# Performance work log

Hardware: AMD Instinct MI355X
Metric: run time of the kernel (lower is better)

Reference implementation:

```python
import jax, jax.numpy as jnp
import numpy as np

V_CNT = 10000
B = 16
N = B * V_CNT          # total nodes
K = 6                  # Chebyshev order
CH = [3, 128, 64, 32, 128]
G = 8                  # GroupNorm groups (divides 128, 64, 32)
EPS = 1e-5
AVG_DEG = 16


def setup_inputs() -> dict:
    key = jax.random.key(0)
    ks = jax.random.split(key, 8)
    n_edges = N * AVG_DEG
    inp = {
        "x": jax.random.normal(ks[0], (N, CH[0]), jnp.float32),
        "edge_index": jax.random.randint(ks[1], (2, n_edges), 0, N, jnp.int32).astype(jnp.int64),
    }
    for l in range(3):
        cin, cout = CH[l], CH[l + 1]
        s = (1.0 / (cin * K)) ** 0.5
        inp[f"W{l}"] = jax.random.uniform(ks[2 + l], (K, cin, cout), jnp.float32, -s, s)
        inp[f"b{l}"] = jnp.zeros((cout,), jnp.float32)
        inp[f"gamma{l}"] = jnp.ones((cout,), jnp.float32)
        inp[f"beta{l}"] = jnp.zeros((cout,), jnp.float32)
    din = V_CNT * CH[3]
    s = (1.0 / din) ** 0.5
    inp["W_last"] = jax.random.uniform(ks[5], (din, CH[4]), jnp.float32, -s, s)
    inp["b_last"] = jnp.zeros((CH[4],), jnp.float32)
    return inp


def _cheb_edge_weights(edge_index):
    # PyG ChebConv sym normalization with lambda_max=2: L_hat = L - I = -D^{-1/2} A D^{-1/2}
    row, col = edge_index[0], edge_index[1]
    deg = jax.ops.segment_sum(jnp.ones(row.shape, jnp.float32), row, num_segments=N)
    dis = jnp.where(deg > 0, jax.lax.rsqrt(jnp.maximum(deg, 1.0)), 0.0)  # deg^{-1/2}, inf->0
    return -dis[row] * dis[col], row, col


def _cheb_conv(x, row, col, w, W, b):
    # Chebyshev recursion: Tx0=x, Tx1=L_hat x, Tx_k = 2 L_hat Tx_{k-1} - Tx_{k-2}
    prop = lambda h: jax.ops.segment_sum(w[:, None] * h[col], row, num_segments=N)
    Tx0 = x
    out = Tx0 @ W[0]
    Tx1 = prop(Tx0)
    out = out + Tx1 @ W[1]
    for k in range(2, W.shape[0]):
        Tx2 = 2.0 * prop(Tx1) - Tx0
        out = out + Tx2 @ W[k]
        Tx0, Tx1 = Tx1, Tx2
    return out + b


def _group_norm(h, gamma, beta):
    n, C = h.shape
    hg = h.reshape(n, G, C // G)
    mu = hg.mean(axis=2, keepdims=True)
    var = hg.var(axis=2, keepdims=True)
    hg = (hg - mu) * jax.lax.rsqrt(var + EPS)
    return hg.reshape(n, C) * gamma + beta


def reference(x, edge_index, W0, b0, gamma0, beta0, W1, b1, gamma1, beta1,
              W2, b2, gamma2, beta2, W_last, b_last):
    w, row, col = _cheb_edge_weights(edge_index)
    Ws = [W0, W1, W2]
    bs = [b0, b1, b2]
    gs = [gamma0, gamma1, gamma2]
    betas = [beta0, beta1, beta2]
    h = x
    for l in range(3):
        h = _cheb_conv(h, row, col, w, Ws[l], bs[l])
        h = _group_norm(h, gs[l], betas[l])
        h = jax.nn.relu(h)
    h = h.reshape(-1, V_CNT * CH[3])  # [B, v_cnt*32]
    return h @ W_last + b_last
```

## Files before the change

kernel.cpp:

```cpp
#include <hip/hip_runtime.h>
#include <hip/hip_fp16.h>


#define NN 160000
#define EE 2560000
#define FD2 256

typedef __attribute__((ext_vector_type(8))) _Float16 half8;
typedef __attribute__((ext_vector_type(4))) float floatx4;

__device__ inline float2 h2f2(unsigned u) {
  __half2 h = __builtin_bit_cast(__half2, u);
  return __half22float2(h);
}
__device__ inline unsigned short f2h(float f) {
  return __builtin_bit_cast(unsigned short, __float2half_rn(f));
}
__device__ inline unsigned packh2(float a, float b) {
  return __builtin_bit_cast(unsigned, __floats2half2_rn(a, b));
}

__global__ __launch_bounds__(256) void k_zero(int* __restrict__ p, int n) {
  int i = blockIdx.x * 256 + threadIdx.x;
  if (i < n) p[i] = 0;
}

__global__ __launch_bounds__(256) void k_hist(const int* __restrict__ ei, int* __restrict__ deg) {
  int e = blockIdx.x * 256 + threadIdx.x;
  if (e < EE) atomicAdd(&deg[ei[e]], 1);
}

__global__ __launch_bounds__(256) void k_dis(const int* __restrict__ deg, float* __restrict__ dis) {
  int i = blockIdx.x * 256 + threadIdx.x;
  if (i < NN) { int d = deg[i]; dis[i] = d > 0 ? rsqrtf((float)d) : 0.f; }
}

__global__ __launch_bounds__(256) void k_scan1(const int* __restrict__ deg, int* __restrict__ rowStart,
                                               int* __restrict__ bsum) {
  __shared__ int s[256];
  int tid = threadIdx.x;
  int i = blockIdx.x * 256 + tid;
  int v = deg[i];
  s[tid] = v;
  __syncthreads();
  for (int off = 1; off < 256; off <<= 1) {
    int t = (tid >= off) ? s[tid - off] : 0;
    __syncthreads();
    s[tid] += t;
    __syncthreads();
  }
  rowStart[i] = s[tid] - v;
  if (tid == 255) bsum[blockIdx.x] = s[255];
}

__global__ void k_scan2(int* __restrict__ bsum, int nb) {
  __shared__ int s[1024];
  int tid = threadIdx.x;
  int v = (tid < nb) ? bsum[tid] : 0;
  s[tid] = v;
  __syncthreads();
  for (int off = 1; off < 1024; off <<= 1) {
    int t = (tid >= off) ? s[tid - off] : 0;
    __syncthreads();
    s[tid] += t;
    __syncthreads();
  }
  if (tid < nb) bsum[tid] = s[tid] - v;
}

__global__ __launch_bounds__(256) void k_scan3(int* __restrict__ rowStart, const int* __restrict__ bsum) {
  int i = blockIdx.x * 256 + threadIdx.x;
  rowStart[i] += bsum[blockIdx.x];
  if (i == 0) rowStart[NN] = EE;
}

__global__ __launch_bounds__(256) void k_scatter(const int* __restrict__ ei, const int* __restrict__ rowStart,
                                                 int* __restrict__ cursor, const float* __restrict__ dis,
                                                 int2* __restrict__ ew) {
  int e = blockIdx.x * 256 + threadIdx.x;
  if (e >= EE) return;
  int r = ei[e];
  int c = ei[EE + e];
  int pos = rowStart[r] + atomicAdd(&cursor[r], 1);
  ew[pos] = make_int2(c, __float_as_int(-dis[r] * dis[c]));
}

__global__ __launch_bounds__(256) void k_copyx(const float* __restrict__ x, float* __restrict__ A,
                                               unsigned short* __restrict__ TxAll) {
  int i = blockIdx.x * 256 + threadIdx.x;
  if (i < NN * 3) {
    float v = x[i];
    A[i] = v;
    int node = i / 3, c = i - node * 3;
    TxAll[node * 32 + c] = f2h(v);
  }
}

template <int MODE>
__global__ __launch_bounds__(256) void k_prop3(const float* __restrict__ Tsrc, float* __restrict__ Tdst,
                                               unsigned short* __restrict__ TxAll, int ks,
                                               const int* __restrict__ rowStart, const int2* __restrict__ ew) {
  int i = blockIdx.x * 256 + threadIdx.x;
  if (i >= NN) return;
  float a0 = 0.f, a1 = 0.f, a2 = 0.f;
  int e = rowStart[i], e1 = rowStart[i + 1];
  for (; e + 3 < e1; e += 4) {
    int2 p0 = ew[e], p1 = ew[e + 1], p2 = ew[e + 2], p3 = ew[e + 3];
    float w0 = __int_as_float(p0.y), w1 = __int_as_float(p1.y);
    float w2 = __int_as_float(p2.y), w3 = __int_as_float(p3.y);
    a0 += w0 * Tsrc[p0.x * 3] + w1 * Tsrc[p1.x * 3] + w2 * Tsrc[p2.x * 3] + w3 * Tsrc[p3.x * 3];
    a1 += w0 * Tsrc[p0.x * 3 + 1] + w1 * Tsrc[p1.x * 3 + 1] + w2 * Tsrc[p2.x * 3 + 1] + w3 * Tsrc[p3.x * 3 + 1];
    a2 += w0 * Tsrc[p0.x * 3 + 2] + w1 * Tsrc[p1.x * 3 + 2] + w2 * Tsrc[p2.x * 3 + 2] + w3 * Tsrc[p3.x * 3 + 2];
  }
  for (; e < e1; e++) {
    int2 p0 = ew[e];
    float w0 = __int_as_float(p0.y);
    a0 += w0 * Tsrc[p0.x * 3];
    a1 += w0 * Tsrc[p0.x * 3 + 1];
    a2 += w0 * Tsrc[p0.x * 3 + 2];
  }
  if (MODE == 2) {
    a0 = 2.f * a0 - Tdst[i * 3];
    a1 = 2.f * a1 - Tdst[i * 3 + 1];
    a2 = 2.f * a2 - Tdst[i * 3 + 2];
  }
  Tdst[i * 3] = a0; Tdst[i * 3 + 1] = a1; Tdst[i * 3 + 2] = a2;
  unsigned short* tp = TxAll + i * 32 + ks * 3;
  tp[0] = f2h(a0); tp[1] = f2h(a1); tp[2] = f2h(a2);
}

__global__ __launch_bounds__(256) void k_padW0(const float* __restrict__ W0, unsigned short* __restrict__ Bt) {
  int idx = blockIdx.x * 256 + threadIdx.x;
  if (idx >= 128 * 32) return;
  int co = idx >> 5, t = idx & 31;
  Bt[co * 32 + t] = (t < 18) ? f2h(W0[t * 128 + co]) : (unsigned short)0;
}

template <int CIN, int COUT>
__global__ __launch_bounds__(256) void k_combine(const float* __restrict__ W, unsigned short* __restrict__ Bt) {
  int idx = blockIdx.x * 256 + threadIdx.x;
  if (idx >= CIN * 6 * COUT) return;
  int co = idx % COUT;
  int j  = (idx / COUT) % 6;
  int ci = idx / (6 * COUT);
  float c0, c1, c2, c3, c4, c5;
  switch (j) {
    case 0:  c0 = 1;  c1 = 0;  c2 = -1; c3 = 0;   c4 = 1;  c5 = 0;   break;
    case 1:  c0 = 0;  c1 = 1;  c2 = 0;  c3 = -3;  c4 = 0;  c5 = 5;   break;
    case 2:  c0 = 0;  c1 = 0;  c2 = 2;  c3 = 0;   c4 = -8; c5 = 0;   break;
    case 3:  c0 = 0;  c1 = 0;  c2 = 0;  c3 = 4;   c4 = 0;  c5 = -20; break;
    case 4:  c0 = 0;  c1 = 0;  c2 = 0;  c3 = 0;   c4 = 8;  c5 = 0;   break;
    default: c0 = 0;  c1 = 0;  c2 = 0;  c3 = 0;   c4 = 0;  c5 = 16;  break;
  }
  float s = 0.f;
  s += c0 * W[(0 * CIN + ci) * COUT + co];
  s += c1 * W[(1 * CIN + ci) * COUT + co];
  s += c2 * W[(2 * CIN + ci) * COUT + co];
  s += c3 * W[(3 * CIN + ci) * COUT + co];
  s += c4 * W[(4 * CIN + ci) * COUT + co];
  s += c5 * W[(5 * CIN + ci) * COUT + co];
  Bt[(j * COUT + co) * CIN + ci] = f2h(s);
}

template <int KDIM, int COUT>
__global__ __launch_bounds__(256) void k_gemm(const unsigned short* __restrict__ A,
                                              const unsigned short* __restrict__ Bt,
                                              unsigned short* __restrict__ Y) {
  constexpr int KP = KDIM + 8;
  __shared__ unsigned short As[64 * KP];
  __shared__ unsigned short Bs[64 * KP];
  int i0 = blockIdx.x * 64;
  int c0 = blockIdx.y * 64;
  for (int idx = threadIdx.x; idx < 64 * (KDIM / 8); idx += 256) {
    int row = idx / (KDIM / 8), seg = idx % (KDIM / 8);
    uint4 v = ((const uint4*)A)[(size_t)(i0 + row) * (KDIM / 8) + seg];
    *reinterpret_cast<uint4*>(&As[row * KP + seg * 8]) = v;
  }
  for (int idx = threadIdx.x; idx < 64 * (KDIM / 8); idx += 256) {
    int row = idx / (KDIM / 8), seg = idx % (KDIM / 8);
    uint4 v = ((const uint4*)Bt)[(size_t)(c0 + row) * (KDIM / 8) + seg];
    *reinterpret_cast<uint4*>(&Bs[row * KP + seg * 8]) = v;
  }
  __syncthreads();
  int w = threadIdx.x >> 6, lane = threadIdx.x & 63;
  int mn = lane & 15, q = lane >> 4;
  floatx4 acc[4];
#pragma unroll
  for (int cb = 0; cb < 4; cb++) acc[cb] = {0.f, 0.f, 0.f, 0.f};
#pragma unroll
  for (int ks = 0; ks < KDIM / 32; ks++) {
    half8 af = *reinterpret_cast<const half8*>(&As[(16 * w + mn) * KP + ks * 32 + q * 8]);
#pragma unroll
    for (int cb = 0; cb < 4; cb++) {
      half8 bf = *reinterpret_cast<const half8*>(&Bs[(cb * 16 + mn) * KP + ks * 32 + q * 8]);
      acc[cb] = __builtin_amdgcn_mfma_f32_16x16x32_f16(af, bf, acc[cb], 0, 0, 0);
    }
  }
#pragma unroll
  for (int cb = 0; cb < 4; cb++) {
    int jc = c0 + cb * 16 + mn;
    int slice = jc / COUT, cc = jc % COUT;
    unsigned short* dst = Y + (size_t)slice * NN * COUT + cc;
#pragma unroll
    for (int r = 0; r < 4; r++) {
      int i = i0 + 16 * w + q * 4 + r;
      dst[(size_t)i * COUT] = f2h(acc[cb][r]);
    }
  }
}

template <int CPN>
__global__ __launch_bounds__(256) void k_horner(const unsigned* __restrict__ Ysrc, unsigned* __restrict__ Ydst,
                                                const int* __restrict__ rowStart, const int2* __restrict__ ew) {
  int t = blockIdx.x * 256 + threadIdx.x;
  int i = t / CPN;
  int cp = t % CPN;
  float2 a = h2f2(Ydst[(size_t)i * CPN + cp]);
  float acc0 = a.x, acc1 = a.y;
  int e = rowStart[i], e1 = rowStart[i + 1];
  for (; e + 7 < e1; e += 8) {
    int2 p[8];
    unsigned u[8];
#pragma unroll
    for (int k = 0; k < 8; k++) p[k] = ew[e + k];
#pragma unroll
    for (int k = 0; k < 8; k++) u[k] = Ysrc[(size_t)p[k].x * CPN + cp];
#pragma unroll
    for (int k = 0; k < 8; k++) {
      float w = __int_as_float(p[k].y);
      float2 f = h2f2(u[k]);
      acc0 += w * f.x;
      acc1 += w * f.y;
    }
  }
  for (; e < e1; e++) {
    int2 p0 = ew[e];
    float w0 = __int_as_float(p0.y);
    float2 f0 = h2f2(Ysrc[(size_t)p0.x * CPN + cp]);
    acc0 += w0 * f0.x;
    acc1 += w0 * f0.y;
  }
  Ydst[(size_t)i * CPN + cp] = packh2(acc0, acc1);
}

template <int CPG>
__global__ __launch_bounds__(256) void k_gn(const unsigned short* __restrict__ src, const float* __restrict__ bias,
                                            const float* __restrict__ gamma, const float* __restrict__ beta,
                                            unsigned short* __restrict__ dst) {
  constexpr int C = CPG * 8;
  int t = blockIdx.x * 256 + threadIdx.x;
  int i = t >> 3, g = t & 7;
  float v[CPG];
  const unsigned* p = reinterpret_cast<const unsigned*>(src + (size_t)i * C + g * CPG);
#pragma unroll
  for (int q = 0; q < CPG / 2; q++) {
    float2 f = h2f2(p[q]);
    v[2 * q] = f.x; v[2 * q + 1] = f.y;
  }
  float mean = 0.f;
#pragma unroll
  for (int c = 0; c < CPG; c++) { v[c] += bias[g * CPG + c]; mean += v[c]; }
  mean *= (1.f / CPG);
  float var = 0.f;
#pragma unroll
  for (int c = 0; c < CPG; c++) { float d = v[c] - mean; var += d * d; }
  var *= (1.f / CPG);
  float rs = rsqrtf(var + 1e-5f);
  unsigned* dp = reinterpret_cast<unsigned*>(dst + (size_t)i * C + g * CPG);
#pragma unroll
  for (int q = 0; q < CPG / 2; q++) {
    float o0 = fmaxf((v[2 * q] - mean) * rs * gamma[g * CPG + 2 * q] + beta[g * CPG + 2 * q], 0.f);
    float o1 = fmaxf((v[2 * q + 1] - mean) * rs * gamma[g * CPG + 2 * q + 1] + beta[g * CPG + 2 * q + 1], 0.f);
    dp[q] = packh2(o0, o1);
  }
}

__global__ __launch_bounds__(256) void k_final1(const unsigned short* __restrict__ h3,
                                                const float* __restrict__ Wl,
                                                float* __restrict__ part) {
  __shared__ float hs[16 * FD2];
  __shared__ float red[2048];
  int d0 = blockIdx.x * FD2;
  const unsigned* h3u = reinterpret_cast<const unsigned*>(h3);
  for (int idx = threadIdx.x; idx < 16 * (FD2 / 2); idx += 256) {
    int b = idx / (FD2 / 2), dq = idx % (FD2 / 2);
    float2 f = h2f2(h3u[(size_t)b * 160000 + (d0 >> 1) + dq]);
    hs[b * FD2 + 2 * dq] = f.x;
    hs[b * FD2 + 2 * dq + 1] = f.y;
  }
  __syncthreads();
  int w = threadIdx.x >> 6, lane = threadIdx.x & 63;
  float a0[16], a1[16];
#pragma unroll
  for (int b = 0; b < 16; b++) { a0[b] = 0.f; a1[b] = 0.f; }
  const float* wp = Wl + (size_t)(d0 + w * (FD2 / 4)) * 128 + 2 * lane;
#pragma unroll 2
  for (int r = 0; r < FD2 / 4; r++) {
    float2 wv = *reinterpret_cast<const float2*>(wp + (size_t)r * 128);
    int row = w * (FD2 / 4) + r;
#pragma unroll
    for (int b = 0; b < 16; b++) {
      float h = hs[b * FD2 + row];
      a0[b] += wv.x * h;
      a1[b] += wv.y * h;
    }
  }
  float2* red2 = reinterpret_cast<float2*>(red);
  for (int ww = 0; ww < 4; ww++) {
    if (w == ww) {
#pragma unroll
      for (int b = 0; b < 16; b++) {
        if (ww == 0) {
          red2[b * 64 + lane] = make_float2(a0[b], a1[b]);
        } else {
          float2 r2 = red2[b * 64 + lane];
          r2.x += a0[b]; r2.y += a1[b];
          red2[b * 64 + lane] = r2;
        }
      }
    }
    __syncthreads();
  }
  for (int i = threadIdx.x; i < 2048; i += 256)
    part[(size_t)blockIdx.x * 2048 + i] = red[i];
}

__global__ __launch_bounds__(256) void k_final2(const float* __restrict__ part, const float* __restrict__ bl,
                                                float* __restrict__ out) {
  int o = blockIdx.x * 256 + threadIdx.x;
  float s = bl[o & 127];
#pragma unroll 10
  for (int p = 0; p < 1250; p++) s += part[(size_t)p * 2048 + o];
  out[o] = s;
}

extern "C" void kernel_launch(void* const* d_in, const int* in_sizes, int n_in,
                              void* d_out, int out_size, void* d_ws, size_t ws_size,
                              hipStream_t stream) {
  const float* x   = (const float*)d_in[0];
  const int*   ei  = (const int*)d_in[1];
  const float* W0  = (const float*)d_in[2];
  const float* b0  = (const float*)d_in[3];
  const float* g0  = (const float*)d_in[4];
  const float* be0 = (const float*)d_in[5];
  const float* W1  = (const float*)d_in[6];
  const float* b1  = (const float*)d_in[7];
  const float* g1  = (const float*)d_in[8];
  const float* be1 = (const float*)d_in[9];
  const float* W2  = (const float*)d_in[10];
  const float* b2  = (const float*)d_in[11];
  const float* g2  = (const float*)d_in[12];
  const float* be2 = (const float*)d_in[13];
  const float* Wl  = (const float*)d_in[14];
  const float* bl  = (const float*)d_in[15];
  float* out = (float*)d_out;
  (void)in_sizes; (void)n_in; (void)out_size; (void)ws_size;

  char* pw = (char*)d_ws;
  auto carve = [&](size_t bytes) -> void* {
    void* r = (void*)pw;
    pw += (bytes + 255) & ~(size_t)255;
    return r;
  };
  int*            deg      = (int*)   carve((size_t)NN * 4);
  int*            cursor   = (int*)   carve((size_t)NN * 4);
  int*            rowStart = (int*)   carve((size_t)(NN + 1) * 4);
  int*            bsum     = (int*)   carve(1024 * 4);
  float*          dis      = (float*) carve((size_t)NN * 4);
  int2*           ew       = (int2*)  carve((size_t)EE * 8);
  unsigned short* Cwt      = (unsigned short*)carve((size_t)384 * 128 * 2);
  unsigned short* TxAll    = (unsigned short*)carve((size_t)NN * 32 * 2);
  float*          A3       = (float*) carve((size_t)NN * 3 * 4);
  float*          B3       = (float*) carve((size_t)NN * 3 * 4);
  unsigned short* Hbuf     = (unsigned short*)carve((size_t)NN * 128 * 2);
  unsigned short* Ybuf     = (unsigned short*)carve((size_t)NN * 384 * 2);
  float*          part     = (float*) carve((size_t)1250 * 2048 * 4);

  k_zero<<<1250, 256, 0, stream>>>(deg, 2 * NN);
  k_hist<<<10000, 256, 0, stream>>>(ei, deg);
  k_dis<<<625, 256, 0, stream>>>(deg, dis);
  k_scan1<<<625, 256, 0, stream>>>(deg, rowStart, bsum);
  k_scan2<<<1, 1024, 0, stream>>>(bsum, 625);
  k_scan3<<<625, 256, 0, stream>>>(rowStart, bsum);
  k_scatter<<<10000, 256, 0, stream>>>(ei, rowStart, cursor, dis, ew);

  k_zero<<<10000, 256, 0, stream>>>((int*)TxAll, NN * 16);
  k_copyx<<<1875, 256, 0, stream>>>(x, A3, TxAll);
  k_prop3<1><<<625, 256, 0, stream>>>(A3, B3, TxAll, 1, rowStart, ew);
  k_prop3<2><<<625, 256, 0, stream>>>(B3, A3, TxAll, 2, rowStart, ew);
  k_prop3<2><<<625, 256, 0, stream>>>(A3, B3, TxAll, 3, rowStart, ew);
  k_prop3<2><<<625, 256, 0, stream>>>(B3, A3, TxAll, 4, rowStart, ew);
  k_prop3<2><<<625, 256, 0, stream>>>(A3, B3, TxAll, 5, rowStart, ew);
  k_padW0<<<16, 256, 0, stream>>>(W0, Cwt);
  k_gemm<32, 128><<<dim3(2500, 2), 256, 0, stream>>>(TxAll, Cwt, Ybuf);
  k_gn<16><<<5000, 256, 0, stream>>>(Ybuf, b0, g0, be0, Hbuf);

  k_combine<128, 64><<<192, 256, 0, stream>>>(W1, Cwt);
  k_gemm<128, 64><<<dim3(2500, 6), 256, 0, stream>>>(Hbuf, Cwt, Ybuf);
  for (int j = 4; j >= 0; j--)
    k_horner<32><<<20000, 256, 0, stream>>>((unsigned*)(Ybuf + (size_t)(j + 1) * NN * 64),
                                            (unsigned*)(Ybuf + (size_t)j * NN * 64), rowStart, ew);
  k_gn<8><<<5000, 256, 0, stream>>>(Ybuf, b1, g1, be1, Hbuf);

  k_combine<64, 32><<<48, 256, 0, stream>>>(W2, Cwt);
  k_gemm<64, 32><<<dim3(2500, 3), 256, 0, stream>>>(Hbuf, Cwt, Ybuf);
  for (int j = 4; j >= 0; j--)
    k_horner<16><<<10000, 256, 0, stream>>>((unsigned*)(Ybuf + (size_t)(j + 1) * NN * 32),
                                            (unsigned*)(Ybuf + (size_t)j * NN * 32), rowStart, ew);
  k_gn<4><<<5000, 256, 0, stream>>>(Ybuf, b2, g2, be2, Hbuf);

  k_final1<<<1250, 256, 0, stream>>>(Hbuf, Wl, part);
  k_final2<<<8, 256, 0, stream>>>(part, bl, out);
}
```

Measured before the change: 1.436 ms.

## Factor symmetric normalization out of edge weights, store column indices only

Replaces the per-edge (col, weight) int2 CSR with a plain column-index array by factoring the weight -dis[r]*dis[c] into row and column scalings. Sources are pre-scaled by dis, both in the 3-channel recursion (with float4-padded buffers) and in the GEMM epilogue and Horner steps for the later layers. This halves the edge-array bandwidth and removes per-edge multiplies in the sparse gathers. In exchange it adds extra scaling passes and changes fp16 rounding, since the pre-scaled values are stored in half precision.

After: 1.477 ms. 1.03x slower.

```diff
diff --git a/kernel.cpp b/kernel.cpp
--- a/kernel.cpp
+++ b/kernel.cpp
@@ -68,63 +68,67 @@
   if (tid < nb) bsum[tid] = s[tid] - v;
 }
 
-__global__ __launch_bounds__(256) void k_scan3(int* __restrict__ rowStart, const int* __restrict__ bsum) {
+__global__ __launch_bounds__(256) void k_scan3(int* __restrict__ rowStart, const int* __restrict__ bsum,
+                                               int* __restrict__ cur) {
   int i = blockIdx.x * 256 + threadIdx.x;
-  rowStart[i] += bsum[blockIdx.x];
+  int v = rowStart[i] + bsum[blockIdx.x];
+  rowStart[i] = v;
+  cur[i] = v;
   if (i == 0) rowStart[NN] = EE;
 }
 
-__global__ __launch_bounds__(256) void k_scatter(const int* __restrict__ ei, const int* __restrict__ rowStart,
-                                                 int* __restrict__ cursor, const float* __restrict__ dis,
-                                                 int2* __restrict__ ew) {
+__global__ __launch_bounds__(256) void k_scatter(const int* __restrict__ ei, int* __restrict__ cur,
+                                                 int* __restrict__ colIdx) {
   int e = blockIdx.x * 256 + threadIdx.x;
   if (e >= EE) return;
   int r = ei[e];
-  int c = ei[EE + e];
-  int pos = rowStart[r] + atomicAdd(&cursor[r], 1);
-  ew[pos] = make_int2(c, __float_as_int(-dis[r] * dis[c]));
-}
-
-__global__ __launch_bounds__(256) void k_copyx(const float* __restrict__ x, float* __restrict__ A,
+  int pos = atomicAdd(&cur[r], 1);
+  colIdx[pos] = ei[EE + e];
+}
+
+__global__ __launch_bounds__(256) void k_copyx(const float* __restrict__ x, const float* __restrict__ dis,
+                                               float4* __restrict__ T, float4* __restrict__ S,
                                                unsigned short* __restrict__ TxAll) {
   int i = blockIdx.x * 256 + threadIdx.x;
-  if (i < NN * 3) {
-    float v = x[i];
-    A[i] = v;
-    int node = i / 3, c = i - node * 3;
-    TxAll[node * 32 + c] = f2h(v);
-  }
+  if (i >= NN) return;
+  float x0 = x[3 * i], x1 = x[3 * i + 1], x2 = x[3 * i + 2];
+  float di = dis[i];
+  T[i] = make_float4(x0, x1, x2, 0.f);
+  S[i] = make_float4(di * x0, di * x1, di * x2, 0.f);
+  unsigned short* tp = TxAll + i * 32;
+  tp[0] = f2h(x0); tp[1] = f2h(x1); tp[2] = f2h(x2);
 }
 
 template <int MODE>
-__global__ __launch_bounds__(256) void k_prop3(const float* __restrict__ Tsrc, float* __restrict__ Tdst,
-                                               unsigned short* __restrict__ TxAll, int ks,
-                                               const int* __restrict__ rowStart, const int2* __restrict__ ew) {
+__global__ __launch_bounds__(256) void k_prop3(const float4* __restrict__ Ssrc, float4* __restrict__ Tdst,
+                                               float4* __restrict__ Sdst, unsigned short* __restrict__ TxAll,
+                                               int ks, const int* __restrict__ rowStart,
+                                               const int* __restrict__ colIdx, const float* __restrict__ dis) {
   int i = blockIdx.x * 256 + threadIdx.x;
   if (i >= NN) return;
-  float a0 = 0.f, a1 = 0.f, a2 = 0.f;
+  float s0 = 0.f, s1 = 0.f, s2 = 0.f;
   int e = rowStart[i], e1 = rowStart[i + 1];
   for (; e + 3 < e1; e += 4) {
-    int2 p0 = ew[e], p1 = ew[e + 1], p2 = ew[e + 2], p3 = ew[e + 3];
-    float w0 = __int_as_float(p0.y), w1 = __int_as_float(p1.y);
-    float w2 = __int_as_float(p2.y), w3 = __int_as_float(p3.y);
-    a0 += w0 * Tsrc[p0.x * 3] + w1 * Tsrc[p1.x * 3] + w2 * Tsrc[p2.x * 3] + w3 * Tsrc[p3.x * 3];
-    a1 += w0 * Tsrc[p0.x * 3 + 1] + w1 * Tsrc[p1.x * 3 + 1] + w2 * Tsrc[p2.x * 3 + 1] + w3 * Tsrc[p3.x * 3 + 1];
-    a2 += w0 * Tsrc[p0.x * 3 + 2] + w1 * Tsrc[p1.x * 3 + 2] + w2 * Tsrc[p2.x * 3 + 2] + w3 * Tsrc[p3.x * 3 + 2];
+    int c0 = colIdx[e], c1 = colIdx[e + 1], c2 = colIdx[e + 2], c3 = colIdx[e + 3];
+    float4 f0 = Ssrc[c0], f1 = Ssrc[c1], f2 = Ssrc[c2], f3 = Ssrc[c3];
+    s0 += f0.x + f1.x + f2.x + f3.x;
+    s1 += f0.y + f1.y + f2.y + f3.y;
+    s2 += f0.z + f1.z + f2.z + f3.z;
   }
   for (; e < e1; e++) {
-    int2 p0 = ew[e];
-    float w0 = __int_as_float(p0.y);
-    a0 += w0 * Tsrc[p0.x * 3];
-    a1 += w0 * Tsrc[p0.x * 3 + 1];
-    a2 += w0 * Tsrc[p0.x * 3 + 2];
-  }
+    float4 f0 = Ssrc[colIdx[e]];
+    s0 += f0.x; s1 += f0.y; s2 += f0.z;
+  }
+  float di = dis[i];
+  float a0 = -di * s0, a1 = -di * s1, a2 = -di * s2;
   if (MODE == 2) {
-    a0 = 2.f * a0 - Tdst[i * 3];
-    a1 = 2.f * a1 - Tdst[i * 3 + 1];
-    a2 = 2.f * a2 - Tdst[i * 3 + 2];
-  }
-  Tdst[i * 3] = a0; Tdst[i * 3 + 1] = a1; Tdst[i * 3 + 2] = a2;
+    float4 tp = Tdst[i];
+    a0 = 2.f * a0 - tp.x;
+    a1 = 2.f * a1 - tp.y;
+    a2 = 2.f * a2 - tp.z;
+  }
+  Tdst[i] = make_float4(a0, a1, a2, 0.f);
+  Sdst[i] = make_float4(di * a0, di * a1, di * a2, 0.f);
   unsigned short* tp = TxAll + i * 32 + ks * 3;
   tp[0] = f2h(a0); tp[1] = f2h(a1); tp[2] = f2h(a2);
 }
@@ -165,6 +169,7 @@
 template <int KDIM, int COUT>
 __global__ __launch_bounds__(256) void k_gemm(const unsigned short* __restrict__ A,
                                               const unsigned short* __restrict__ Bt,
+                                              const float* __restrict__ dis, int scaleFrom,
                                               unsigned short* __restrict__ Y) {
   constexpr int KP = KDIM + 8;
   __shared__ unsigned short As[64 * KP];
@@ -196,6 +201,9 @@
       acc[cb] = __builtin_amdgcn_mfma_f32_16x16x32_f16(af, bf, acc[cb], 0, 0, 0);
     }
   }
+  float dv[4];
+#pragma unroll
+  for (int r = 0; r < 4; r++) dv[r] = dis[i0 + 16 * w + q * 4 + r];
 #pragma unroll
   for (int cb = 0; cb < 4; cb++) {
     int jc = c0 + cb * 16 + mn;
@@ -204,43 +212,44 @@
 #pragma unroll
     for (int r = 0; r < 4; r++) {
       int i = i0 + 16 * w + q * 4 + r;
-      dst[(size_t)i * COUT] = f2h(acc[cb][r]);
+      float sc = (slice >= scaleFrom) ? dv[r] : 1.f;
+      dst[(size_t)i * COUT] = f2h(acc[cb][r] * sc);
     }
   }
 }
 
 template <int CPN>
 __global__ __launch_bounds__(256) void k_horner(const unsigned* __restrict__ Ysrc, unsigned* __restrict__ Ydst,
-                                                const int* __restrict__ rowStart, const int2* __restrict__ ew) {
+                                                const int* __restrict__ rowStart, const int* __restrict__ colIdx,
+                                                const float* __restrict__ dis, int isFinal) {
   int t = blockIdx.x * 256 + threadIdx.x;
   int i = t / CPN;
   int cp = t % CPN;
-  float2 a = h2f2(Ydst[(size_t)i * CPN + cp]);
-  float acc0 = a.x, acc1 = a.y;
+  float acc0 = 0.f, acc1 = 0.f;
   int e = rowStart[i], e1 = rowStart[i + 1];
   for (; e + 7 < e1; e += 8) {
-    int2 p[8];
+    int cA[8];
+#pragma unroll
+    for (int k = 0; k < 8; k++) cA[k] = colIdx[e + k];
     unsigned u[8];
 #pragma unroll
-    for (int k = 0; k < 8; k++) p[k] = ew[e + k];
-#pragma unroll
-    for (int k = 0; k < 8; k++) u[k] = Ysrc[(size_t)p[k].x * CPN + cp];
+    for (int k = 0; k < 8; k++) u[k] = Ysrc[(size_t)cA[k] * CPN + cp];
 #pragma unroll
     for (int k = 0; k < 8; k++) {
-      float w = __int_as_float(p[k].y);
       float2 f = h2f2(u[k]);
-      acc0 += w * f.x;
-      acc1 += w * f.y;
+      acc0 += f.x;
+      acc1 += f.y;
     }
   }
   for (; e < e1; e++) {
-    int2 p0 = ew[e];
-    float w0 = __int_as_float(p0.y);
-    float2 f0 = h2f2(Ysrc[(size_t)p0.x * CPN + cp]);
-    acc0 += w0 * f0.x;
-    acc1 += w0 * f0.y;
-  }
-  Ydst[(size_t)i * CPN + cp] = packh2(acc0, acc1);
+    float2 f = h2f2(Ysrc[(size_t)colIdx[e] * CPN + cp]);
+    acc0 += f.x;
+    acc1 += f.y;
+  }
+  float di = dis[i];
+  float coef = isFinal ? di : di * di;
+  float2 y = h2f2(Ydst[(size_t)i * CPN + cp]);
+  Ydst[(size_t)i * CPN + cp] = packh2(y.x - coef * acc0, y.y - coef * acc1);
 }
 
 template <int CPG>
@@ -363,50 +372,54 @@
     return r;
   };
   int*            deg      = (int*)   carve((size_t)NN * 4);
-  int*            cursor   = (int*)   carve((size_t)NN * 4);
+  int*            cur      = (int*)   carve((size_t)NN * 4);
   int*            rowStart = (int*)   carve((size_t)(NN + 1) * 4);
   int*            bsum     = (int*)   carve(1024 * 4);
   float*          dis      = (float*) carve((size_t)NN * 4);
-  int2*           ew       = (int2*)  carve((size_t)EE * 8);
+  int*            colIdx   = (int*)   carve((size_t)EE * 4);
   unsigned short* Cwt      = (unsigned short*)carve((size_t)384 * 128 * 2);
   unsigned short* TxAll    = (unsigned short*)carve((size_t)NN * 32 * 2);
-  float*          A3       = (float*) carve((size_t)NN * 3 * 4);
-  float*          B3       = (float*) carve((size_t)NN * 3 * 4);
+  float4*         T_A      = (float4*)carve((size_t)NN * 16);
+  float4*         T_B      = (float4*)carve((size_t)NN * 16);
+  float4*         S_A      = (float4*)carve((size_t)NN * 16);
+  float4*         S_B      = (float4*)carve((size_t)NN * 16);
   unsigned short* Hbuf     = (unsigned short*)carve((size_t)NN * 128 * 2);
   unsigned short* Ybuf     = (unsigned short*)carve((size_t)NN * 384 * 2);
   float*          part     = (float*) carve((size_t)1250 * 2048 * 4);
 
-  k_zero<<<1250, 256, 0, stream>>>(deg, 2 * NN);
+  k_zero<<<625, 256, 0, stream>>>(deg, NN);
   k_hist<<<10000, 256, 0, stream>>>(ei, deg);
   k_dis<<<625, 256, 0, stream>>>(deg, dis);
   k_scan1<<<625, 256, 0, stream>>>(deg, rowStart, bsum);
   k_scan2<<<1, 1024, 0, stream>>>(bsum, 625);
-  k_scan3<<<625, 256, 0, stream>>>(rowStart, bsum);
-  k_scatter<<<10000, 256, 0, stream>>>(ei, rowStart, cursor, dis, ew);
+  k_scan3<<<625, 256, 0, stream>>>(rowStart, bsum, cur);
+  k_scatter<<<10000, 256, 0, stream>>>(ei, cur, colIdx);
 
   k_zero<<<10000, 256, 0, stream>>>((int*)TxAll, NN * 16);
-  k_copyx<<<1875, 256, 0, stream>>>(x, A3, TxAll);
-  k_prop3<1><<<625, 256, 0, stream>>>(A3, B3, TxAll, 1, rowStart, ew);
-  k_prop3<2><<<625, 256, 0, stream>>>(B3, A3, TxAll, 2, rowStart, ew);
-  k_prop3<2><<<625, 256, 0, stream>>>(A3, B3, TxAll, 3, rowStart, ew);
-  k_prop3<2><<<625, 256, 0, stream>>>(B3, A3, TxAll, 4, rowStart, ew);
-  k_prop3<2><<<625, 256, 0, stream>>>(A3, B3, TxAll, 5, rowStart, ew);
+  k_copyx<<<625, 256, 0, stream>>>(x, dis, T_A, S_A, TxAll);
+  k_prop3<1><<<625, 256, 0, stream>>>(S_A, T_B, S_B, TxAll, 1, rowStart, colIdx, dis);
+  k_prop3<2><<<625, 256, 0, stream>>>(S_B, T_A, S_A, TxAll, 2, rowStart, colIdx, dis);
+  k_prop3<2><<<625, 256, 0, stream>>>(S_A, T_B, S_B, TxAll, 3, rowStart, colIdx, dis);
+  k_prop3<2><<<625, 256, 0, stream>>>(S_B, T_A, S_A, TxAll, 4, rowStart, colIdx, dis);
+  k_prop3<2><<<625, 256, 0, stream>>>(S_A, T_B, S_B, TxAll, 5, rowStart, colIdx, dis);
   k_padW0<<<16, 256, 0, stream>>>(W0, Cwt);
-  k_gemm<32, 128><<<dim3(2500, 2), 256, 0, stream>>>(TxAll, Cwt, Ybuf);
+  k_gemm<32, 128><<<dim3(2500, 2), 256, 0, stream>>>(TxAll, Cwt, dis, 99, Ybuf);
   k_gn<16><<<5000, 256, 0, stream>>>(Ybuf, b0, g0, be0, Hbuf);
 
   k_combine<128, 64><<<192, 256, 0, stream>>>(W1, Cwt);
-  k_gemm<128, 64><<<dim3(2500, 6), 256, 0, stream>>>(Hbuf, Cwt, Ybuf);
+  k_gemm<128, 64><<<dim3(2500, 6), 256, 0, stream>>>(Hbuf, Cwt, dis, 1, Ybuf);
   for (int j = 4; j >= 0; j--)
     k_horner<32><<<20000, 256, 0, stream>>>((unsigned*)(Ybuf + (size_t)(j + 1) * NN * 64),
-                                            (unsigned*)(Ybuf + (size_t)j * NN * 64), rowStart, ew);
+                                            (unsigned*)(Ybuf + (size_t)j * NN * 64),
+                                            rowStart, colIdx, dis, j == 0);
   k_gn<8><<<5000, 256, 0, stream>>>(Ybuf, b1, g1, be1, Hbuf);
 
   k_combine<64, 32><<<48, 256, 0, stream>>>(W2, Cwt);
-  k_gemm<64, 32><<<dim3(2500, 3), 256, 0, stream>>>(Hbuf, Cwt, Ybuf);
+  k_gemm<64, 32><<<dim3(2500, 3), 256, 0, stream>>>(Hbuf, Cwt, dis, 1, Ybuf);
   for (int j = 4; j >= 0; j--)
     k_horner<16><<<10000, 256, 0, stream>>>((unsigned*)(Ybuf + (size_t)(j + 1) * NN * 32),
-                                            (unsigned*)(Ybuf + (size_t)j * NN * 32), rowStart, ew);
+                                            (unsigned*)(Ybuf + (size_t)j * NN * 32),
+                                            rowStart, colIdx, dis, j == 0);
   k_gn<4><<<5000, 256, 0, stream>>>(Ybuf, b2, g2, be2, Hbuf);
 
   k_final1<<<1250, 256, 0, stream>>>(Hbuf, Wl, part);
```
